# Kernel optimization log

Measured on AMD Instinct MI355X. Metric: run time of the kernel, lower is better.

The kernel has to match this reference:

```python
import jax, jax.numpy as jnp
import numpy as np

TEMPERATURE = 0.1
GAMMA = 0.5
LOSS_WEIGHT = 1.0
MAX_BATCH_SIZE = 5000
POS_DIST_THRESH = 1.0
NEG_SAMPLE_RATIO = 2.0
EPS_NORM = 1e-8   # torch cosine_similarity norm clamp
EPS_POS = 1e-6


def setup_inputs() -> dict:
    key = jax.random.key(0)
    k1, k2 = jax.random.split(key)
    N, D = 15000, 64
    features = jax.random.normal(k1, (N, D), dtype=jnp.float32)
    # xyz coords in a 20-unit box -> ~8 positive neighbors per point at thresh 1.0
    coords = jax.random.uniform(k2, (N, 3), dtype=jnp.float32) * 20.0
    # all points are power-line class (label 2) so M = N statically
    labels = jnp.full((N,), 2, dtype=jnp.int32)
    return {"features": features, "labels": labels, "coords": coords}


def reference(features, labels, coords):
    # labels are all == 2 and none == ignore_index, so the boolean selections
    # (ignore_index filter, line_mask) are identities: line_feats = features.
    M = features.shape[0]
    # row-normalized features for cosine similarity (torch eps=1e-8 clamp)
    fnorm = features / jnp.maximum(
        jnp.linalg.norm(features, axis=1, keepdims=True), EPS_NORM)
    sq = jnp.sum(coords * coords, axis=1)  # [M]

    total_nce = jnp.float32(0.0)
    total_cont = jnp.float32(0.0)
    col = jnp.arange(M)[None, :]
    for start in range(0, M, MAX_BATCH_SIZE):
        end = min(start + MAX_BATCH_SIZE, M)
        B = end - start
        # [B, M] pairwise cosine similarity
        feat_sim = fnorm[start:end] @ fnorm.T
        # [B, M] euclidean cdist via ||a||^2 + ||b||^2 - 2 a.b
        d2 = sq[start:end, None] + sq[None, :] - 2.0 * (coords[start:end] @ coords.T)
        coord_dist = jnp.sqrt(jnp.maximum(d2, 0.0))
        pos = (coord_dist < POS_DIST_THRESH) & (coord_dist > 1e-6)
        posf = pos.astype(feat_sim.dtype)
        negf = 1.0 - posf

        exp_sim = jnp.exp(feat_sim / TEMPERATURE)
        # k = min(int(neg_sample_ratio * max positives per row), M); traced scalar
        max_neg = (NEG_SAMPLE_RATIO * pos.sum(axis=1).max()).astype(jnp.int32)
        k = jnp.minimum(max_neg, M)
        # top-k sum of masked negatives: full descending sort + length-k row mask
        vals = jnp.sort(exp_sim * negf, axis=1)[:, ::-1]
        sum_exp = jnp.sum(jnp.where(col < k, vals, 0.0), axis=1)

        pos_sum = jnp.sum(exp_sim * posf, axis=1)
        batch_nce = jnp.mean(-jnp.log(pos_sum / (sum_exp + pos_sum + EPS_POS)))
        batch_cont = jnp.mean(jnp.abs((1.0 - feat_sim) - coord_dist) * posf)

        total_nce = total_nce + batch_nce * B
        total_cont = total_cont + batch_cont * B

    loss = (total_nce / M + GAMMA * (total_cont / M)) * LOSS_WEIGHT
    return loss
```

## Files before the change

kernel.cpp:

```cpp
#include <hip/hip_runtime.h>
#include <math.h>

#define NPTS 15000
#define NPAD 15360
#define DIM 64
#define BATCH 5000
#define QT 64
#define NCH 4
#define NBLKQ 235
#define NGB (NBLKQ * NCH)
#define NPB 1875
#define BLKM 512
#define NT (NPAD / 16)
#define NTC (NT / NCH)
#define CAPE 12
#define CAPP 64
#define NCELL 8000
#define NBIN 320
#define HW 160
#define GHW ((size_t)NBLKQ * QT * HW)
#define T_G 0.26f
#define KEY_BASE 0x3E80u

typedef __attribute__((ext_vector_type(8))) short bf16x8;
typedef __attribute__((ext_vector_type(4))) float f32x4;

__device__ __forceinline__ float bf2f(unsigned u) {
  return __uint_as_float(u << 16);
}

__device__ __forceinline__ int cell_xyz(float x, float y, float z) {
  int cx = min(19, max(0, (int)x));
  int cy = min(19, max(0, (int)y));
  int cz = min(19, max(0, (int)z));
  return cx + 20 * (cy + 20 * cz);
}

__global__ __launch_bounds__(1024) void k_norm_cells(const float* __restrict__ feat,
                                                     const float* __restrict__ coords,
                                                     unsigned short* __restrict__ fbf,
                                                     float4* __restrict__ c4,
                                                     float* __restrict__ inv_m,
                                                     uint4* __restrict__ ghist4,
                                                     int* __restrict__ batch_max,
                                                     float* __restrict__ out,
                                                     int* __restrict__ cell_start,
                                                     int* __restrict__ cell_cnt,
                                                     int* __restrict__ pts) {
  __shared__ struct { int cnt[NCELL]; int ptr[NCELL]; int sw[16]; } sc;
  int bx = blockIdx.x, tid = threadIdx.x;
  int lane = tid & 63, wv = tid >> 6;
  unsigned gz = (unsigned)bx * 1024u + (unsigned)tid;
  if (gz < (unsigned)(GHW / 4)) ghist4[gz] = make_uint4(0, 0, 0, 0);
  if (gz == 0) { out[0] = 0.0f; batch_max[0] = 0; batch_max[1] = 0; batch_max[2] = 0; }

  if (bx < 960) {
    int i = bx * 16 + wv;
    int d = lane;
    float v = (i < NPTS) ? feat[i * DIM + d] : 0.0f;
    float ss = v * v;
#pragma unroll
    for (int off = 32; off; off >>= 1) ss += __shfl_down(ss, off);
    ss = __shfl(ss, 0);
    float m = fmaxf(sqrtf(ss), 1e-8f);
    float nv = v / m;
    unsigned u = __float_as_uint(nv);
    fbf[i * DIM + d] = (unsigned short)((u + 0x7FFFu + ((u >> 16) & 1u)) >> 16);
    if (d == 0) {
      float cx = (i < NPTS) ? coords[i * 3] : 0.0f;
      float cy = (i < NPTS) ? coords[i * 3 + 1] : 0.0f;
      float cz = (i < NPTS) ? coords[i * 3 + 2] : 0.0f;
      c4[i] = make_float4(cx, cy, cz, cx * cx + cy * cy + cz * cz);
      if (i < NPTS) inv_m[i] = 1.0f / m;
    }
  } else {
    for (int x = tid; x < NCELL; x += 1024) sc.cnt[x] = 0;
    __syncthreads();
    for (int i = tid; i < NPTS; i += 1024)
      atomicAdd(&sc.cnt[cell_xyz(coords[i * 3], coords[i * 3 + 1], coords[i * 3 + 2])], 1);
    __syncthreads();
    int run = 0;
    for (int c = 0; c < NCELL; c += 1024) {
      int idx = c + tid;
      int v = (idx < NCELL) ? sc.cnt[idx] : 0;
      int inc = v;
#pragma unroll
      for (int off = 1; off < 64; off <<= 1) {
        int o = __shfl_up(inc, off);
        if (lane >= off) inc += o;
      }
      if (lane == 63) sc.sw[wv] = inc;
      __syncthreads();
      int woff = 0, tot = 0;
#pragma unroll
      for (int w = 0; w < 16; ++w) {
        int s = sc.sw[w];
        if (w < wv) woff += s;
        tot += s;
      }
      __syncthreads();
      int excl = run + woff + inc - v;
      if (idx < NCELL) {
        cell_start[idx] = excl;
        cell_cnt[idx] = v;
        sc.ptr[idx] = excl;
      }
      run += tot;
    }
    __syncthreads();
    for (int i = tid; i < NPTS; i += 1024) {
      int ix = atomicAdd(&sc.ptr[cell_xyz(coords[i * 3], coords[i * 3 + 1], coords[i * 3 + 2])], 1);
      pts[ix] = i;
    }
  }
}

union SMem {
  unsigned hist[QT * HW];
  struct {
    int np[8]; int ec[8]; int pc[8];
    int list[8][CAPP];
    float d2s[8][CAPP];
    unsigned short ek[8][CAPE];
  } p;
};

#define LOADT(lo, hi, tt) {                                            \
    const unsigned short* _p = fbf + (size_t)(tt) * 1024 + laneOff;    \
    lo = *(const bf16x8*)_p; hi = *(const bf16x8*)(_p + 32); }

#define PHASE(lo, hi, tn) {                                            \
    f32x4 acc0 = {0,0,0,0}, acc1 = {0,0,0,0},                          \
          acc2 = {0,0,0,0}, acc3 = {0,0,0,0};                          \
    acc0 = __builtin_amdgcn_mfma_f32_16x16x32_bf16(aL[0], lo, acc0, 0, 0, 0); \
    acc0 = __builtin_amdgcn_mfma_f32_16x16x32_bf16(aH[0], hi, acc0, 0, 0, 0); \
    acc1 = __builtin_amdgcn_mfma_f32_16x16x32_bf16(aL[1], lo, acc1, 0, 0, 0); \
    acc1 = __builtin_amdgcn_mfma_f32_16x16x32_bf16(aH[1], hi, acc1, 0, 0, 0); \
    acc2 = __builtin_amdgcn_mfma_f32_16x16x32_bf16(aL[2], lo, acc2, 0, 0, 0); \
    acc2 = __builtin_amdgcn_mfma_f32_16x16x32_bf16(aH[2], hi, acc2, 0, 0, 0); \
    acc3 = __builtin_amdgcn_mfma_f32_16x16x32_bf16(aL[3], lo, acc3, 0, 0, 0); \
    acc3 = __builtin_amdgcn_mfma_f32_16x16x32_bf16(aH[3], hi, acc3, 0, 0, 0); \
    LOADT(lo, hi, tn);                                                 \
    _Pragma("unroll")                                                  \
    for (int r = 0; r < 4; ++r) {                                      \
      float s0 = acc0[r], s1 = acc1[r], s2 = acc2[r], s3 = acc3[r];    \
      int qb = quad * 4 + r;                                           \
      if (s0 >= T_G) {                                                 \
        unsigned bin = (__float_as_uint(s0) >> 16) - KEY_BASE;         \
        atomicAdd(&sm.hist[qb * HW + (bin >> 1)], 1u << ((bin & 1) << 4)); } \
      if (s1 >= T_G) {                                                 \
        unsigned bin = (__float_as_uint(s1) >> 16) - KEY_BASE;         \
        atomicAdd(&sm.hist[(16 + qb) * HW + (bin >> 1)], 1u << ((bin & 1) << 4)); } \
      if (s2 >= T_G) {                                                 \
        unsigned bin = (__float_as_uint(s2) >> 16) - KEY_BASE;         \
        atomicAdd(&sm.hist[(32 + qb) * HW + (bin >> 1)], 1u << ((bin & 1) << 4)); } \
      if (s3 >= T_G) {                                                 \
        unsigned bin = (__float_as_uint(s3) >> 16) - KEY_BASE;         \
        atomicAdd(&sm.hist[(48 + qb) * HW + (bin >> 1)], 1u << ((bin & 1) << 4)); } \
    } }

__global__ __launch_bounds__(BLKM, 4) void k_main(const unsigned short* __restrict__ fbf,
                                                  const float* __restrict__ feat,
                                                  const float* __restrict__ inv_m,
                                                  const float4* __restrict__ c4,
                                                  const int* __restrict__ cell_start,
                                                  const int* __restrict__ cell_cnt,
                                                  const int* __restrict__ pts,
                                                  unsigned* __restrict__ ghist,
                                                  float* __restrict__ g_ps,
                                                  float* __restrict__ row_cont,
                                                  int* __restrict__ batch_max,
                                                  unsigned short* __restrict__ excl_keys,
                                                  int* __restrict__ excl_cnt) {
  __shared__ SMem sm;
  int bx = blockIdx.x;
  int tid = threadIdx.x;
  int wv = tid >> 6, lane = tid & 63;

  if (bx < NGB) {
    int tile = bx >> 2, ch = bx & 3;
    int i0 = tile * QT;
    int l15 = lane & 15, quad = lane >> 4;
    int laneOff = l15 * DIM + quad * 8;

    for (int x = tid; x < QT * HW; x += BLKM) sm.hist[x] = 0;

    bf16x8 aL[4], aH[4];
#pragma unroll
    for (int m = 0; m < 4; ++m) {
      const unsigned short* qrow = fbf + (size_t)(i0 + m * 16 + l15) * DIM + quad * 8;
      aL[m] = *(const bf16x8*)qrow;
      aH[m] = *(const bf16x8*)(qrow + 32);
    }
    __syncthreads();

    int tEnd = (ch + 1) * NTC;
    int t0 = ch * NTC + wv;
    bf16x8 b0L, b0H, b1L, b1H;
    LOADT(b0L, b0H, t0);
    LOADT(b1L, b1H, t0 + 8);
#pragma unroll 1
    for (int k = 0; k < 15; ++k) {
      int t = t0 + k * 16;
      int nA = t + 16, nB = t + 24;
      if (nA >= tEnd) nA = t0;
      if (nB >= tEnd) nB = t0;
      PHASE(b0L, b0H, nA)
      PHASE(b1L, b1H, nB)
    }
    __syncthreads();

    unsigned* gh = ghist + (size_t)i0 * HW;
    for (int x = tid; x < QT * HW; x += BLKM) {
      unsigned v = sm.hist[x];
      if (v) atomicAdd(&gh[x], v);
    }
  } else {
    int bp = bx - NGB;
    int i = bp * 8 + wv;
    if (lane == 0) { sm.p.np[wv] = 0; sm.p.ec[wv] = 0; }
    float4 ci = c4[i];
    int cx = min(19, max(0, (int)ci.x));
    int cy = min(19, max(0, (int)ci.y));
    int cz = min(19, max(0, (int)ci.z));
    if (lane < 27) {
      int gx = cx + lane % 3 - 1, gy = cy + (lane / 3) % 3 - 1, gz = cz + lane / 9 - 1;
      if (gx >= 0 && gx < 20 && gy >= 0 && gy < 20 && gz >= 0 && gz < 20) {
        int cell = gx + 20 * (gy + 20 * gz);
        int s0 = cell_start[cell], e0 = s0 + cell_cnt[cell];
        for (int p = s0; p < e0; ++p) {
          int j = pts[p];
          if (j == i) continue;
          float4 cj = c4[j];
          float ddx = ci.x - cj.x, ddy = ci.y - cj.y, ddz = ci.z - cj.z;
          float d2 = ddx * ddx + ddy * ddy + ddz * ddz;
          if (d2 < 1.0f) {
            int slot = atomicAdd(&sm.p.np[wv], 1);
            if (slot < CAPP) { sm.p.list[wv][slot] = j; sm.p.d2s[wv][slot] = d2; }
          }
        }
      }
    }
    int npt = sm.p.np[wv];
    int np = min(npt, CAPP);
    float psum = 0.f, csum = 0.f;
    if (lane < np) {
      int j = sm.p.list[wv][lane];
      float d2 = sm.p.d2s[wv][lane];
      const float4* fi4 = (const float4*)(feat + (size_t)i * DIM);
      const float4* fj4 = (const float4*)(feat + (size_t)j * DIM);
      float dot = 0.f;
#pragma unroll
      for (int c = 0; c < 16; ++c) {
        float4 a = fi4[c];
        float4 b = fj4[c];
        dot = fmaf(a.w, b.w, fmaf(a.z, b.z, fmaf(a.y, b.y, fmaf(a.x, b.x, dot))));
      }
      dot *= inv_m[i] * inv_m[j];
      psum = expf(dot * 10.0f);
      csum = fabsf((1.0f - dot) - sqrtf(d2));
      if (dot >= T_G) {
        int ix = atomicAdd(&sm.p.ec[wv], 1);
        if (ix < CAPE) sm.p.ek[wv][ix] = (unsigned short)(__float_as_uint(dot) >> 16);
      }
    }
#pragma unroll
    for (int off = 32; off; off >>= 1) {
      psum += __shfl_down(psum, off);
      csum += __shfl_down(csum, off);
    }
    int ec = min(sm.p.ec[wv], CAPE);
    if (lane == 0) {
      g_ps[i] = psum;
      row_cont[i] = csum;
      excl_cnt[i] = ec;
      sm.p.pc[wv] = npt;
    }
    for (int x = lane; x < ec; x += 64) excl_keys[(size_t)i * CAPE + x] = sm.p.ek[wv][x];
    __syncthreads();
    if (tid == 0) {
      int m = 0;
#pragma unroll
      for (int w = 0; w < 8; ++w) m = max(m, sm.p.pc[w]);
      atomicMax(&batch_max[(bp * 8) / BATCH], m);
    }
  }
}

__global__ __launch_bounds__(BLKM) void k_select(const unsigned* __restrict__ ghist,
                                                 const float* __restrict__ g_ps,
                                                 const float* __restrict__ row_cont,
                                                 const int* __restrict__ batch_max,
                                                 const unsigned short* __restrict__ excl_keys,
                                                 const int* __restrict__ excl_cnt,
                                                 float* __restrict__ out) {
  int i0 = blockIdx.x * QT;
  int tid = threadIdx.x;
  int wv = tid >> 6, lane = tid & 63;
  float a_acc = 0.f, b_acc = 0.f;

  for (int qq = 0; qq < 8; ++qq) {
    int iq = i0 + wv * 8 + qq;
    if (iq >= NPTS) continue;
    int kq = min((int)(2.0f * (float)batch_max[iq / BATCH]), NPTS);
    int e = 5 * lane;
    const unsigned* hw_ = ghist + (size_t)iq * HW + (e >> 1);
    unsigned w0 = hw_[0], w1 = hw_[1], w2 = hw_[2];
    bool odd = (lane & 1) != 0;
    int h0 = (int)(odd ? (w0 >> 16) : (w0 & 0xFFFFu));
    int h1 = (int)(odd ? (w1 & 0xFFFFu) : (w0 >> 16));
    int h2 = (int)(odd ? (w1 >> 16) : (w1 & 0xFFFFu));
    int h3 = (int)(odd ? (w2 & 0xFFFFu) : (w1 >> 16));
    int h4 = (int)(odd ? (w2 >> 16) : (w2 & 0xFFFFu));
    int ec = min(excl_cnt[iq], CAPE);
    for (int ee = 0; ee < ec; ++ee) {
      unsigned key = excl_keys[(size_t)iq * CAPE + ee];
      unsigned bin = key - KEY_BASE;
      if (bin > NBIN - 1u) bin = NBIN - 1u;
      int c = (int)bin - e;
      if (c == 0) h0 = max(h0 - 1, 0);
      else if (c == 1) h1 = max(h1 - 1, 0);
      else if (c == 2) h2 = max(h2 - 1, 0);
      else if (c == 3) h3 = max(h3 - 1, 0);
      else if (c == 4) h4 = max(h4 - 1, 0);
    }
    int lsum = h0 + h1 + h2 + h3 + h4;
    int pre = lsum;
#pragma unroll
    for (int off = 1; off < 64; off <<= 1) {
      int o = __shfl_up(pre, off);
      if (lane >= off) pre += o;
    }
    int total = __shfl(pre, 63);
    int tke = min(kq, total);
    int cum = total - pre;
    float se = 0.0f;
    unsigned kb = KEY_BASE + (unsigned)e;
    {
      int tk4 = min(max(tke - cum, 0), h4); cum += h4;
      int tk3 = min(max(tke - cum, 0), h3); cum += h3;
      int tk2 = min(max(tke - cum, 0), h2); cum += h2;
      int tk1 = min(max(tke - cum, 0), h1); cum += h1;
      int tk0 = min(max(tke - cum, 0), h0);
      if (tk4) se += (float)tk4 * expf(10.0f * bf2f(kb + 4));
      if (tk3) se += (float)tk3 * expf(10.0f * bf2f(kb + 3));
      if (tk2) se += (float)tk2 * expf(10.0f * bf2f(kb + 2));
      if (tk1) se += (float)tk1 * expf(10.0f * bf2f(kb + 1));
      if (tk0) se += (float)tk0 * expf(10.0f * bf2f(kb + 0));
    }
#pragma unroll
    for (int off = 32; off; off >>= 1) se += __shfl_down(se, off);
    if (lane == 0) {
      float ps = g_ps[iq];
      float nce = -logf(ps / (se + ps + 1e-6f));
      if (!(nce < 1e30f)) nce = 0.0f;
      a_acc += nce;
      b_acc += row_cont[iq];
    }
  }
  __shared__ float sa[8], sb[8];
  if (lane == 0) { sa[wv] = a_acc; sb[wv] = b_acc; }
  __syncthreads();
  if (tid == 0) {
    float a = 0.f, b = 0.f;
#pragma unroll
    for (int w = 0; w < 8; ++w) { a += sa[w]; b += sb[w]; }
    atomicAdd(out, a / 15000.0f + 0.5f * ((b / 15000.0f) / 15000.0f));
  }
}

extern "C" void kernel_launch(void* const* d_in, const int* in_sizes, int n_in,
                              void* d_out, int out_size, void* d_ws, size_t ws_size,
                              hipStream_t stream) {
  const float* feat   = (const float*)d_in[0];
  const float* coords = (const float*)d_in[2];
  float* out = (float*)d_out;

  char* ws              = (char*)d_ws;
  unsigned short* fbf   = (unsigned short*)ws;
  float4* c4            = (float4*)(fbf + NPAD * DIM);
  float* row_cont       = (float*)(c4 + NPAD);
  float* g_ps           = row_cont + NPTS;
  int*   excl_ct        = (int*)(g_ps + NPTS);
  unsigned short* exclk = (unsigned short*)(excl_ct + NPTS);
  int*   batch_max      = (int*)(exclk + (size_t)NPTS * CAPE);
  float* inv_m          = (float*)(batch_max + 4);
  unsigned* ghist       = (unsigned*)(inv_m + NPTS);
  int*   cell_start     = (int*)(ghist + GHW);
  int*   cell_cnt       = cell_start + NCELL;
  int*   pts            = cell_cnt + NCELL;

  k_norm_cells<<<dim3(961), dim3(1024), 0, stream>>>(feat, coords, fbf, c4, inv_m,
                                                     (uint4*)ghist, batch_max, out,
                                                     cell_start, cell_cnt, pts);
  k_main<<<dim3(NGB + NPB), dim3(BLKM), 0, stream>>>(fbf, feat, inv_m, c4,
                                                     cell_start, cell_cnt, pts,
                                                     ghist, g_ps, row_cont, batch_max,
                                                     exclk, excl_ct);
  k_select<<<dim3(NBLKQ), dim3(BLKM), 0, stream>>>(ghist, g_ps, row_cont, batch_max,
                                                   exclk, excl_ct, out);
}
```

Measured before the change: 188.9 us.

## Fuse top-k selection into main kernel with per-tile full-row shared histograms

Each similarity block now handles 32 query rows over all columns, so the row histogram stays in shared memory. This removes the global histogram buffer, its zeroing, the global atomics that merged chunk results, and the separate select kernel. Blocks that find positive pairs run first and signal completion through a global counter. The histogram blocks spin-wait on that counter before the selection step. This relies on the positive-pair blocks being scheduled ahead of the spinning blocks, which risks deadlock or stalls. It also halves the A-tile reuse per B-tile load.

```diff
diff --git a/kernel.cpp b/kernel.cpp
--- a/kernel.cpp
+++ b/kernel.cpp
@@ -5,20 +5,16 @@
 #define NPAD 15360
 #define DIM 64
 #define BATCH 5000
-#define QT 64
-#define NCH 4
-#define NBLKQ 235
-#define NGB (NBLKQ * NCH)
-#define NPB 1875
-#define BLKM 512
+#define QT 32
+#define NGBL 469
+#define NPBL 938
+#define BLKM 1024
 #define NT (NPAD / 16)
-#define NTC (NT / NCH)
 #define CAPE 12
 #define CAPP 64
 #define NCELL 8000
 #define NBIN 320
 #define HW 160
-#define GHW ((size_t)NBLKQ * QT * HW)
 #define T_G 0.26f
 #define KEY_BASE 0x3E80u
 
@@ -41,8 +37,8 @@
                                                      unsigned short* __restrict__ fbf,
                                                      float4* __restrict__ c4,
                                                      float* __restrict__ inv_m,
-                                                     uint4* __restrict__ ghist4,
                                                      int* __restrict__ batch_max,
+                                                     int* __restrict__ pos_done,
                                                      float* __restrict__ out,
                                                      int* __restrict__ cell_start,
                                                      int* __restrict__ cell_cnt,
@@ -50,9 +46,11 @@
   __shared__ struct { int cnt[NCELL]; int ptr[NCELL]; int sw[16]; } sc;
   int bx = blockIdx.x, tid = threadIdx.x;
   int lane = tid & 63, wv = tid >> 6;
-  unsigned gz = (unsigned)bx * 1024u + (unsigned)tid;
-  if (gz < (unsigned)(GHW / 4)) ghist4[gz] = make_uint4(0, 0, 0, 0);
-  if (gz == 0) { out[0] = 0.0f; batch_max[0] = 0; batch_max[1] = 0; batch_max[2] = 0; }
+  if (bx == 0 && tid == 0) {
+    out[0] = 0.0f;
+    batch_max[0] = 0; batch_max[1] = 0; batch_max[2] = 0;
+    pos_done[0] = 0;
+  }
 
   if (bx < 960) {
     int i = bx * 16 + wv;
@@ -118,10 +116,10 @@
 union SMem {
   unsigned hist[QT * HW];
   struct {
-    int np[8]; int ec[8]; int pc[8];
-    int list[8][CAPP];
-    float d2s[8][CAPP];
-    unsigned short ek[8][CAPE];
+    int np[16]; int ec[16]; int pc[16];
+    int list[16][CAPP];
+    float d2s[16][CAPP];
+    unsigned short ek[16][CAPE];
   } p;
 };
 
@@ -130,20 +128,15 @@
     lo = *(const bf16x8*)_p; hi = *(const bf16x8*)(_p + 32); }
 
 #define PHASE(lo, hi, tn) {                                            \
-    f32x4 acc0 = {0,0,0,0}, acc1 = {0,0,0,0},                          \
-          acc2 = {0,0,0,0}, acc3 = {0,0,0,0};                          \
+    f32x4 acc0 = {0,0,0,0}, acc1 = {0,0,0,0};                          \
     acc0 = __builtin_amdgcn_mfma_f32_16x16x32_bf16(aL[0], lo, acc0, 0, 0, 0); \
     acc0 = __builtin_amdgcn_mfma_f32_16x16x32_bf16(aH[0], hi, acc0, 0, 0, 0); \
     acc1 = __builtin_amdgcn_mfma_f32_16x16x32_bf16(aL[1], lo, acc1, 0, 0, 0); \
     acc1 = __builtin_amdgcn_mfma_f32_16x16x32_bf16(aH[1], hi, acc1, 0, 0, 0); \
-    acc2 = __builtin_amdgcn_mfma_f32_16x16x32_bf16(aL[2], lo, acc2, 0, 0, 0); \
-    acc2 = __builtin_amdgcn_mfma_f32_16x16x32_bf16(aH[2], hi, acc2, 0, 0, 0); \
-    acc3 = __builtin_amdgcn_mfma_f32_16x16x32_bf16(aL[3], lo, acc3, 0, 0, 0); \
-    acc3 = __builtin_amdgcn_mfma_f32_16x16x32_bf16(aH[3], hi, acc3, 0, 0, 0); \
     LOADT(lo, hi, tn);                                                 \
     _Pragma("unroll")                                                  \
     for (int r = 0; r < 4; ++r) {                                      \
-      float s0 = acc0[r], s1 = acc1[r], s2 = acc2[r], s3 = acc3[r];    \
+      float s0 = acc0[r], s1 = acc1[r];                                \
       int qb = quad * 4 + r;                                           \
       if (s0 >= T_G) {                                                 \
         unsigned bin = (__float_as_uint(s0) >> 16) - KEY_BASE;         \
@@ -151,79 +144,37 @@
       if (s1 >= T_G) {                                                 \
         unsigned bin = (__float_as_uint(s1) >> 16) - KEY_BASE;         \
         atomicAdd(&sm.hist[(16 + qb) * HW + (bin >> 1)], 1u << ((bin & 1) << 4)); } \
-      if (s2 >= T_G) {                                                 \
-        unsigned bin = (__float_as_uint(s2) >> 16) - KEY_BASE;         \
-        atomicAdd(&sm.hist[(32 + qb) * HW + (bin >> 1)], 1u << ((bin & 1) << 4)); } \
-      if (s3 >= T_G) {                                                 \
-        unsigned bin = (__float_as_uint(s3) >> 16) - KEY_BASE;         \
-        atomicAdd(&sm.hist[(48 + qb) * HW + (bin >> 1)], 1u << ((bin & 1) << 4)); } \
     } }
 
-__global__ __launch_bounds__(BLKM, 4) void k_main(const unsigned short* __restrict__ fbf,
-                                                  const float* __restrict__ feat,
-                                                  const float* __restrict__ inv_m,
-                                                  const float4* __restrict__ c4,
-                                                  const int* __restrict__ cell_start,
-                                                  const int* __restrict__ cell_cnt,
-                                                  const int* __restrict__ pts,
-                                                  unsigned* __restrict__ ghist,
-                                                  float* __restrict__ g_ps,
-                                                  float* __restrict__ row_cont,
-                                                  int* __restrict__ batch_max,
-                                                  unsigned short* __restrict__ excl_keys,
-                                                  int* __restrict__ excl_cnt) {
+__global__ __launch_bounds__(BLKM) void k_main(const unsigned short* __restrict__ fbf,
+                                               const float* __restrict__ feat,
+                                               const float* __restrict__ inv_m,
+                                               const float4* __restrict__ c4,
+                                               const int* __restrict__ cell_start,
+                                               const int* __restrict__ cell_cnt,
+                                               const int* __restrict__ pts,
+                                               float* __restrict__ g_ps,
+                                               float* __restrict__ row_cont,
+                                               int* __restrict__ batch_max,
+                                               unsigned short* __restrict__ excl_keys,
+                                               int* __restrict__ excl_cnt,
+                                               int* __restrict__ pos_done,
+                                               float* __restrict__ out) {
   __shared__ SMem sm;
+  __shared__ float sa[16], sb[16];
   int bx = blockIdx.x;
   int tid = threadIdx.x;
   int wv = tid >> 6, lane = tid & 63;
 
-  if (bx < NGB) {
-    int tile = bx >> 2, ch = bx & 3;
-    int i0 = tile * QT;
-    int l15 = lane & 15, quad = lane >> 4;
-    int laneOff = l15 * DIM + quad * 8;
-
-    for (int x = tid; x < QT * HW; x += BLKM) sm.hist[x] = 0;
-
-    bf16x8 aL[4], aH[4];
-#pragma unroll
-    for (int m = 0; m < 4; ++m) {
-      const unsigned short* qrow = fbf + (size_t)(i0 + m * 16 + l15) * DIM + quad * 8;
-      aL[m] = *(const bf16x8*)qrow;
-      aH[m] = *(const bf16x8*)(qrow + 32);
-    }
-    __syncthreads();
-
-    int tEnd = (ch + 1) * NTC;
-    int t0 = ch * NTC + wv;
-    bf16x8 b0L, b0H, b1L, b1H;
-    LOADT(b0L, b0H, t0);
-    LOADT(b1L, b1H, t0 + 8);
-#pragma unroll 1
-    for (int k = 0; k < 15; ++k) {
-      int t = t0 + k * 16;
-      int nA = t + 16, nB = t + 24;
-      if (nA >= tEnd) nA = t0;
-      if (nB >= tEnd) nB = t0;
-      PHASE(b0L, b0H, nA)
-      PHASE(b1L, b1H, nB)
-    }
-    __syncthreads();
-
-    unsigned* gh = ghist + (size_t)i0 * HW;
-    for (int x = tid; x < QT * HW; x += BLKM) {
-      unsigned v = sm.hist[x];
-      if (v) atomicAdd(&gh[x], v);
-    }
-  } else {
-    int bp = bx - NGB;
-    int i = bp * 8 + wv;
+  if (bx < NPBL) {
+    int i = bx * 16 + wv;
+    bool valid = (i < NPTS);
     if (lane == 0) { sm.p.np[wv] = 0; sm.p.ec[wv] = 0; }
     float4 ci = c4[i];
     int cx = min(19, max(0, (int)ci.x));
     int cy = min(19, max(0, (int)ci.y));
     int cz = min(19, max(0, (int)ci.z));
-    if (lane < 27) {
+    if (valid && lane < 27) {
       int gx = cx + lane % 3 - 1, gy = cy + (lane / 3) % 3 - 1, gz = cz + lane / 9 - 1;
       if (gx >= 0 && gx < 20 && gy >= 0 && gy < 20 && gz >= 0 && gz < 20) {
         int cell = gx + 20 * (gy + 20 * gz);
@@ -244,7 +195,7 @@
     int npt = sm.p.np[wv];
     int np = min(npt, CAPP);
     float psum = 0.f, csum = 0.f;
-    if (lane < np) {
+    if (valid && lane < np) {
       int j = sm.p.list[wv][lane];
       float d2 = sm.p.d2s[wv][lane];
       const float4* fi4 = (const float4*)(feat + (size_t)i * DIM);
@@ -269,103 +220,139 @@
       psum += __shfl_down(psum, off);
       csum += __shfl_down(csum, off);
     }
-    int ec = min(sm.p.ec[wv], CAPE);
-    if (lane == 0) {
+    int ec = valid ? min(sm.p.ec[wv], CAPE) : 0;
+    if (valid && lane == 0) {
       g_ps[i] = psum;
       row_cont[i] = csum;
       excl_cnt[i] = ec;
-      sm.p.pc[wv] = npt;
     }
     for (int x = lane; x < ec; x += 64) excl_keys[(size_t)i * CAPE + x] = sm.p.ek[wv][x];
+    if (lane == 0) sm.p.pc[wv] = valid ? npt : 0;
     __syncthreads();
     if (tid == 0) {
-      int m = 0;
-#pragma unroll
-      for (int w = 0; w < 8; ++w) m = max(m, sm.p.pc[w]);
-      atomicMax(&batch_max[(bp * 8) / BATCH], m);
-    }
-  }
-}
-
-__global__ __launch_bounds__(BLKM) void k_select(const unsigned* __restrict__ ghist,
-                                                 const float* __restrict__ g_ps,
-                                                 const float* __restrict__ row_cont,
-                                                 const int* __restrict__ batch_max,
-                                                 const unsigned short* __restrict__ excl_keys,
-                                                 const int* __restrict__ excl_cnt,
-                                                 float* __restrict__ out) {
-  int i0 = blockIdx.x * QT;
-  int tid = threadIdx.x;
-  int wv = tid >> 6, lane = tid & 63;
-  float a_acc = 0.f, b_acc = 0.f;
-
-  for (int qq = 0; qq < 8; ++qq) {
-    int iq = i0 + wv * 8 + qq;
-    if (iq >= NPTS) continue;
-    int kq = min((int)(2.0f * (float)batch_max[iq / BATCH]), NPTS);
-    int e = 5 * lane;
-    const unsigned* hw_ = ghist + (size_t)iq * HW + (e >> 1);
-    unsigned w0 = hw_[0], w1 = hw_[1], w2 = hw_[2];
-    bool odd = (lane & 1) != 0;
-    int h0 = (int)(odd ? (w0 >> 16) : (w0 & 0xFFFFu));
-    int h1 = (int)(odd ? (w1 & 0xFFFFu) : (w0 >> 16));
-    int h2 = (int)(odd ? (w1 >> 16) : (w1 & 0xFFFFu));
-    int h3 = (int)(odd ? (w2 & 0xFFFFu) : (w1 >> 16));
-    int h4 = (int)(odd ? (w2 >> 16) : (w2 & 0xFFFFu));
-    int ec = min(excl_cnt[iq], CAPE);
-    for (int ee = 0; ee < ec; ++ee) {
-      unsigned key = excl_keys[(size_t)iq * CAPE + ee];
-      unsigned bin = key - KEY_BASE;
-      if (bin > NBIN - 1u) bin = NBIN - 1u;
-      int c = (int)bin - e;
-      if (c == 0) h0 = max(h0 - 1, 0);
-      else if (c == 1) h1 = max(h1 - 1, 0);
-      else if (c == 2) h2 = max(h2 - 1, 0);
-      else if (c == 3) h3 = max(h3 - 1, 0);
-      else if (c == 4) h4 = max(h4 - 1, 0);
-    }
-    int lsum = h0 + h1 + h2 + h3 + h4;
-    int pre = lsum;
-#pragma unroll
-    for (int off = 1; off < 64; off <<= 1) {
-      int o = __shfl_up(pre, off);
-      if (lane >= off) pre += o;
-    }
-    int total = __shfl(pre, 63);
-    int tke = min(kq, total);
-    int cum = total - pre;
-    float se = 0.0f;
-    unsigned kb = KEY_BASE + (unsigned)e;
-    {
-      int tk4 = min(max(tke - cum, 0), h4); cum += h4;
-      int tk3 = min(max(tke - cum, 0), h3); cum += h3;
-      int tk2 = min(max(tke - cum, 0), h2); cum += h2;
-      int tk1 = min(max(tke - cum, 0), h1); cum += h1;
-      int tk0 = min(max(tke - cum, 0), h0);
-      if (tk4) se += (float)tk4 * expf(10.0f * bf2f(kb + 4));
-      if (tk3) se += (float)tk3 * expf(10.0f * bf2f(kb + 3));
-      if (tk2) se += (float)tk2 * expf(10.0f * bf2f(kb + 2));
-      if (tk1) se += (float)tk1 * expf(10.0f * bf2f(kb + 1));
-      if (tk0) se += (float)tk0 * expf(10.0f * bf2f(kb + 0));
-    }
-#pragma unroll
-    for (int off = 32; off; off >>= 1) se += __shfl_down(se, off);
-    if (lane == 0) {
-      float ps = g_ps[iq];
-      float nce = -logf(ps / (se + ps + 1e-6f));
-      if (!(nce < 1e30f)) nce = 0.0f;
-      a_acc += nce;
-      b_acc += row_cont[iq];
-    }
-  }
-  __shared__ float sa[8], sb[8];
-  if (lane == 0) { sa[wv] = a_acc; sb[wv] = b_acc; }
-  __syncthreads();
-  if (tid == 0) {
-    float a = 0.f, b = 0.f;
-#pragma unroll
-    for (int w = 0; w < 8; ++w) { a += sa[w]; b += sb[w]; }
-    atomicAdd(out, a / 15000.0f + 0.5f * ((b / 15000.0f) / 15000.0f));
+      int curb = -1, curm = 0;
+      for (int w = 0; w < 16; ++w) {
+        int iw = bx * 16 + w;
+        if (iw >= NPTS) break;
+        int b = iw / BATCH;
+        if (b != curb) {
+          if (curb >= 0 && curm > 0) atomicMax(&batch_max[curb], curm);
+          curb = b; curm = 0;
+        }
+        curm = max(curm, sm.p.pc[w]);
+      }
+      if (curb >= 0 && curm > 0) atomicMax(&batch_max[curb], curm);
+      __threadfence();
+      atomicAdd(pos_done, 1);
+    }
+  } else {
+    int tile = bx - NPBL;
+    int i0 = tile * QT;
+    int l15 = lane & 15, quad = lane >> 4;
+    int laneOff = l15 * DIM + quad * 8;
+
+    for (int x = tid; x < QT * HW; x += BLKM) sm.hist[x] = 0;
+
+    bf16x8 aL[2], aH[2];
+#pragma unroll
+    for (int m = 0; m < 2; ++m) {
+      const unsigned short* qrow = fbf + (size_t)(i0 + m * 16 + l15) * DIM + quad * 8;
+      aL[m] = *(const bf16x8*)qrow;
+      aH[m] = *(const bf16x8*)(qrow + 32);
+    }
+    __syncthreads();
+
+    int t0 = wv;
+    bf16x8 b0L, b0H, b1L, b1H;
+    LOADT(b0L, b0H, t0);
+    LOADT(b1L, b1H, t0 + 16);
+#pragma unroll 1
+    for (int k = 0; k < 30; ++k) {
+      int t = t0 + k * 32;
+      int nA = t + 32, nB = t + 48;
+      if (nA >= NT) nA = t0;
+      if (nB >= NT) nB = t0;
+      PHASE(b0L, b0H, nA)
+      PHASE(b1L, b1H, nB)
+    }
+    __syncthreads();
+
+    if (tid == 0) {
+      while (atomicAdd(pos_done, 0) < NPBL) __builtin_amdgcn_s_sleep(64);
+      __threadfence();
+    }
+    __syncthreads();
+
+    float a_acc = 0.f, b_acc = 0.f;
+#pragma unroll
+    for (int qq = 0; qq < 2; ++qq) {
+      int q = wv * 2 + qq;
+      int iq = i0 + q;
+      if (iq >= NPTS) continue;
+      int kq = min((int)(2.0f * (float)batch_max[iq / BATCH]), NPTS);
+      int e = 5 * lane;
+      const unsigned* hwp = &sm.hist[q * HW + (e >> 1)];
+      unsigned w0 = hwp[0], w1 = hwp[1], w2 = hwp[2];
+      bool odd = (lane & 1) != 0;
+      int h0 = (int)(odd ? (w0 >> 16) : (w0 & 0xFFFFu));
+      int h1 = (int)(odd ? (w1 & 0xFFFFu) : (w0 >> 16));
+      int h2 = (int)(odd ? (w1 >> 16) : (w1 & 0xFFFFu));
+      int h3 = (int)(odd ? (w2 & 0xFFFFu) : (w1 >> 16));
+      int h4 = (int)(odd ? (w2 >> 16) : (w2 & 0xFFFFu));
+      int ec = min(excl_cnt[iq], CAPE);
+      for (int ee = 0; ee < ec; ++ee) {
+        unsigned key = excl_keys[(size_t)iq * CAPE + ee];
+        unsigned bin = key - KEY_BASE;
+        if (bin > NBIN - 1u) bin = NBIN - 1u;
+        int c = (int)bin - e;
+        if (c == 0) h0 = max(h0 - 1, 0);
+        else if (c == 1) h1 = max(h1 - 1, 0);
+        else if (c == 2) h2 = max(h2 - 1, 0);
+        else if (c == 3) h3 = max(h3 - 1, 0);
+        else if (c == 4) h4 = max(h4 - 1, 0);
+      }
+      int lsum = h0 + h1 + h2 + h3 + h4;
+      int pre = lsum;
+#pragma unroll
+      for (int off = 1; off < 64; off <<= 1) {
+        int o = __shfl_up(pre, off);
+        if (lane >= off) pre += o;
+      }
+      int total = __shfl(pre, 63);
+      int tke = min(kq, total);
+      int cum = total - pre;
+      float se = 0.0f;
+      unsigned kb = KEY_BASE + (unsigned)e;
+      {
+        int tk4 = min(max(tke - cum, 0), h4); cum += h4;
+        int tk3 = min(max(tke - cum, 0), h3); cum += h3;
+        int tk2 = min(max(tke - cum, 0), h2); cum += h2;
+        int tk1 = min(max(tke - cum, 0), h1); cum += h1;
+        int tk0 = min(max(tke - cum, 0), h0);
+        if (tk4) se += (float)tk4 * expf(10.0f * bf2f(kb + 4));
+        if (tk3) se += (float)tk3 * expf(10.0f * bf2f(kb + 3));
+        if (tk2) se += (float)tk2 * expf(10.0f * bf2f(kb + 2));
+        if (tk1) se += (float)tk1 * expf(10.0f * bf2f(kb + 1));
+        if (tk0) se += (float)tk0 * expf(10.0f * bf2f(kb + 0));
+      }
+#pragma unroll
+      for (int off = 32; off; off >>= 1) se += __shfl_down(se, off);
+      if (lane == 0) {
+        float ps = g_ps[iq];
+        float nce = -logf(ps / (se + ps + 1e-6f));
+        if (!(nce < 1e30f)) nce = 0.0f;
+        a_acc += nce;
+        b_acc += row_cont[iq];
+      }
+    }
+    if (lane == 0) { sa[wv] = a_acc; sb[wv] = b_acc; }
+    __syncthreads();
+    if (tid == 0) {
+      float a = 0.f, b = 0.f;
+#pragma unroll
+      for (int w = 0; w < 16; ++w) { a += sa[w]; b += sb[w]; }
+      atomicAdd(out, a / 15000.0f + 0.5f * ((b / 15000.0f) / 15000.0f));
+    }
   }
 }
 
@@ -384,19 +371,17 @@
   int*   excl_ct        = (int*)(g_ps + NPTS);
   unsigned short* exclk = (unsigned short*)(excl_ct + NPTS);
   int*   batch_max      = (int*)(exclk + (size_t)NPTS * CAPE);
-  float* inv_m          = (float*)(batch_max + 4);
-  unsigned* ghist       = (unsigned*)(inv_m + NPTS);
-  int*   cell_start     = (int*)(ghist + GHW);
+  int*   pos_done       = batch_max + 4;
+  float* inv_m          = (float*)(pos_done + 4);
+  int*   cell_start     = (int*)(inv_m + NPTS);
   int*   cell_cnt       = cell_start + NCELL;
   int*   pts            = cell_cnt + NCELL;
 
   k_norm_cells<<<dim3(961), dim3(1024), 0, stream>>>(feat, coords, fbf, c4, inv_m,
-                                                     (uint4*)ghist, batch_max, out,
+                                                     batch_max, pos_done, out,
                                                      cell_start, cell_cnt, pts);
-  k_main<<<dim3(NGB + NPB), dim3(BLKM), 0, stream>>>(fbf, feat, inv_m, c4,
-                                                     cell_start, cell_cnt, pts,
-                                                     ghist, g_ps, row_cont, batch_max,
-                                                     exclk, excl_ct);
-  k_select<<<dim3(NBLKQ), dim3(BLKM), 0, stream>>>(ghist, g_ps, row_cont, batch_max,
-                                                   exclk, excl_ct, out);
-}
+  k_main<<<dim3(NPBL + NGBL), dim3(BLKM), 0, stream>>>(fbf, feat, inv_m, c4,
+                                                       cell_start, cell_cnt, pts,
+                                                       g_ps, row_cont, batch_max,
+                                                       exclk, excl_ct, pos_done, out);
+}
```

Measured after the change: 263.9 us. 39.7% more time.
